# Optimization experiments

Measured on AMD Instinct MI355X. Metric: run time of the kernel, lower is better.

## Reference

```python
import jax, jax.numpy as jnp
import numpy as np

BEV_H, BEV_W, BEV_Z = 100, 100, 4
PC_RANGE = (-51.2, -51.2, -5.0, 51.2, 51.2, 3.0)
EPS = 1e-5
N_CAM, C_DIM, H_IMG, W_IMG, BATCH = 6, 256, 32, 88, 1


def _make_lidar2img(n_cam, h_img, w_img):
    # Realistic rig: n_cam cameras at equal yaw spacing, ~70 deg HFOV,
    # intrinsics expressed in feature-map pixel units.
    fx = w_img / (2.0 * np.tan(np.deg2rad(35.0)))
    fy = fx
    cx, cy = w_img / 2.0, h_img / 2.0
    K = np.array([[fx, 0, cx, 0], [0, fy, cy, 0], [0, 0, 1, 0], [0, 0, 0, 1]], np.float32)
    mats = []
    for i in range(n_cam):
        th = 2.0 * np.pi * i / n_cam
        c, s = np.cos(th), np.sin(th)
        # camera: z forward (world yaw th), x right, y down; camera at ego origin
        R = np.array([[-s, c, 0.0], [0.0, 0.0, -1.0], [c, s, 0.0]], np.float32)
        T = np.eye(4, dtype=np.float32)
        T[:3, :3] = R
        mats.append(K @ T)
    return np.stack(mats)[None]  # (1, n_cam, 4, 4)


def get_reference_points(H, W, Z, bs):
    ref_y, ref_x = jnp.meshgrid(
        jnp.linspace(0.5, H - 0.5, H, dtype=jnp.float32),
        jnp.linspace(0.5, W - 0.5, W, dtype=jnp.float32), indexing='ij')
    ref_y = (ref_y.reshape(-1) / H)[None, :, None]          # (1, HW, 1)
    ref_x = (ref_x.reshape(-1) / W)[None, :, None]
    ref_x = jnp.broadcast_to(ref_x, (1, H * W, Z))
    ref_y = jnp.broadcast_to(ref_y, (1, H * W, Z))
    ref_z = jnp.broadcast_to(jnp.linspace(0.5, Z - 0.5, Z, dtype=jnp.float32)[None, None, :], (1, H * W, Z))
    ref_3d = jnp.stack((ref_x, ref_y, ref_z), -1)           # (1, HW, Z, 3)
    return jnp.broadcast_to(ref_3d, (bs, H * W, Z, 3))


def bilinear_sample(img, gx, gy):
    # img: (BN, C, H, W); gx, gy in [-1, 1]: (BN, P)
    # F.grid_sample bilinear, padding_mode='zeros', align_corners=False
    BN, C, H, W = img.shape
    x = (gx + 1.0) * W * 0.5 - 0.5
    y = (gy + 1.0) * H * 0.5 - 0.5
    x0 = jnp.floor(x)
    y0 = jnp.floor(y)
    wx1 = x - x0
    wy1 = y - y0
    flat = img.reshape(BN, C, H * W)

    def corner(xi, yi, w):
        valid = (xi >= 0) & (xi < W) & (yi >= 0) & (yi < H)
        xc = jnp.clip(xi, 0, W - 1).astype(jnp.int32)
        yc = jnp.clip(yi, 0, H - 1).astype(jnp.int32)
        idx = yc * W + xc                                   # (BN, P)
        idx = jnp.broadcast_to(idx[:, None, :], (BN, C, idx.shape[-1]))
        vals = jnp.take_along_axis(flat, idx, axis=2)       # (BN, C, P)
        return vals * (w * valid.astype(img.dtype))[:, None, :]

    out = corner(x0, y0, (1 - wx1) * (1 - wy1))
    out = out + corner(x0 + 1, y0, wx1 * (1 - wy1))
    out = out + corner(x0, y0 + 1, (1 - wx1) * wy1)
    out = out + corner(x0 + 1, y0 + 1, wx1 * wy1)
    return out


def setup_inputs() -> dict:
    key = jax.random.key(0)
    k0, k1, k2, k3 = jax.random.split(key, 4)
    Nq = BEV_H * BEV_W
    query = jax.random.normal(k0, (BATCH, Nq, C_DIM), jnp.float32)
    img_feats = jax.random.normal(k1, (BATCH, N_CAM, C_DIM, H_IMG, W_IMG), jnp.float32)
    lidar2img = jnp.asarray(_make_lidar2img(N_CAM, H_IMG, W_IMG))
    W_out = jax.random.normal(k2, (C_DIM, C_DIM), jnp.float32) * 0.02
    b_out = jax.random.normal(k3, (C_DIM,), jnp.float32) * 0.02
    return {'query': query, 'img_feats': img_feats, 'lidar2img': lidar2img,
            'W_out': W_out, 'b_out': b_out}


def reference(query, img_feats, lidar2img, W_out, b_out):
    B, Nq, C = query.shape
    N_cam, _, H_img, W_img = img_feats.shape[1], img_feats.shape[2], img_feats.shape[3], img_feats.shape[4]
    Z = BEV_Z
    pc = PC_RANGE

    ref = get_reference_points(BEV_H, BEV_W, Z, B)          # (B, Nq, Z, 3) normalized
    ref = jnp.stack([
        ref[..., 0] * (pc[3] - pc[0]) + pc[0],
        ref[..., 1] * (pc[4] - pc[1]) + pc[1],
        ref[..., 2] * (pc[5] - pc[2]) + pc[2],
    ], axis=-1)
    pts = jnp.concatenate([ref, jnp.ones_like(ref[..., :1])], -1)  # (B, Nq, Z, 4)
    pts = pts.reshape(B, Nq * Z, 4)
    # project: (B, N_cam, P, 4)
    cam = jnp.einsum('bnij,bpj->bnpi', lidar2img, pts)
    z = cam[..., 2:3]
    mask = z > EPS
    xy = cam[..., 0:2] / jnp.maximum(z, EPS)
    gx = (xy[..., 0] / W_img - 0.5) * 2.0                    # (B, N_cam, P)
    gy = (xy[..., 1] / H_img - 0.5) * 2.0
    mask = (mask[..., 0] & (gx > -1.0) & (gx < 1.0) & (gy > -1.0) & (gy < 1.0))

    img_flat = img_feats.reshape(B * N_cam, C, H_img, W_img)
    sampled = bilinear_sample(img_flat, gx.reshape(B * N_cam, -1), gy.reshape(B * N_cam, -1))
    sampled = sampled.reshape(B, N_cam, C, Nq, Z)
    sampled = jnp.nan_to_num(sampled * mask.reshape(B, N_cam, 1, Nq, Z).astype(sampled.dtype))

    w = jnp.mean(sampled, axis=1)                            # (B, C, Nq, Z) mean over cams
    w = jnp.mean(w, axis=3)                                  # (B, C, Nq) mean over Z
    out = jnp.transpose(w, (0, 2, 1))                        # (B, Nq, C)
    return out @ W_out.T + b_out + query
```

## Files before the change

### kernel.cpp

```cpp
#include <hip/hip_runtime.h>
#include <hip/hip_bf16.h>
#include <math.h>

#define BEV_H 100
#define BEV_W 100
#define BEV_Z 4
#define N_CAM 6
#define C_DIM 256
#define H_IMG 32
#define W_IMG 88
#define NQ (BEV_H * BEV_W)
#define HW_IMG (H_IMG * W_IMG)

typedef float f32x4 __attribute__((ext_vector_type(4)));
typedef short short8 __attribute__((ext_vector_type(8)));

__device__ __forceinline__ unsigned short f2b(float f) {
    __hip_bfloat16 h = __float2bfloat16(f);
    return *reinterpret_cast<unsigned short*>(&h);
}
__device__ __forceinline__ float b2f_lo(unsigned int u) {
    return __uint_as_float(u << 16);
}
__device__ __forceinline__ float b2f_hi(unsigned int u) {
    return __uint_as_float(u & 0xffff0000u);
}

__device__ __forceinline__ int xcd_swz(int bid, int nwg) {
    int q = nwg >> 3, r = nwg & 7;
    int xcd = bid & 7;
    int idx = bid >> 3;
    int base = (xcd < r) ? xcd * (q + 1) : r * (q + 1) + (xcd - r) * q;
    return base + idx;
}

__global__ __launch_bounds__(256) void prep_kernel(const float* __restrict__ img,
                                                   const float* __restrict__ Wout,
                                                   unsigned short* __restrict__ imgT,
                                                   unsigned short* __restrict__ Woutb) {
    int cam = blockIdx.z;
    int t = threadIdx.x;
    if (cam == N_CAM) {
        if (blockIdx.y == 0 && blockIdx.x < 64) {
            int base = (blockIdx.x * 256 + t) * 4;
            float4 v = *(const float4*)(Wout + base);
            ushort4 o;
            o.x = f2b(v.x); o.y = f2b(v.y); o.z = f2b(v.z); o.w = f2b(v.w);
            *(ushort4*)(Woutb + base) = o;
        }
        return;
    }
    __shared__ unsigned short tile[32][68];
    int hw0 = blockIdx.x * 32;
    int c0  = blockIdx.y * 64;
    const float* src = img + (size_t)cam * C_DIM * HW_IMG;
    #pragma unroll
    for (int i = 0; i < 2; ++i) {
        int e = i * 256 + t;
        int c  = e >> 3;
        int hq = e & 7;
        float4 v = *(const float4*)(src + (size_t)(c0 + c) * HW_IMG + hw0 + hq * 4);
        tile[hq * 4 + 0][c] = f2b(v.x);
        tile[hq * 4 + 1][c] = f2b(v.y);
        tile[hq * 4 + 2][c] = f2b(v.z);
        tile[hq * 4 + 3][c] = f2b(v.w);
    }
    __syncthreads();
    unsigned short* dst = imgT + (size_t)cam * HW_IMG * C_DIM;
    #pragma unroll
    for (int i = 0; i < 2; ++i) {
        int e = i * 256 + t;
        int hw = e >> 4;
        int cq = e & 15;
        ushort4 o;
        o.x = tile[hw][cq * 4 + 0];
        o.y = tile[hw][cq * 4 + 1];
        o.z = tile[hw][cq * 4 + 2];
        o.w = tile[hw][cq * 4 + 3];
        *(ushort4*)(dst + (size_t)(hw0 + hw) * C_DIM + c0 + cq * 4) = o;
    }
}

__global__ __launch_bounds__(256) void sample_kernel(const unsigned short* __restrict__ imgT,
                                                     const float* __restrict__ l2i,
                                                     unsigned short* __restrict__ wbuf) {
    __shared__ int   ent_off[8][24][4];
    __shared__ float ent_w[8][24][4];
    __shared__ int   counts[8];
    int t = threadIdx.x;
    int blk = xcd_swz(blockIdx.x, NQ / 8);

    {
        int ql   = t >> 5;
        int slot = t & 31;
        int q = blk * 8 + ql;
        int ix = q % BEV_W;
        int iy = q / BEV_W;
        float x = ((ix + 0.5f) / (float)BEV_W) * 102.4f - 51.2f;
        float y = ((iy + 0.5f) / (float)BEV_H) * 102.4f - 51.2f;

        bool valid = false;
        int   o0 = 0, o1 = 0, o2 = 0, o3 = 0;
        float w0 = 0.f, w1 = 0.f, w2 = 0.f, w3 = 0.f;
        if (slot < 24) {
            int cam = slot >> 2;
            int zi  = slot & 3;
            const float* L = l2i + cam * 16;
            float zl = (zi + 0.5f) * 8.0f - 5.0f;
            float cx = fmaf(L[0], x, fmaf(L[1], y, fmaf(L[2],  zl, L[3])));
            float cy = fmaf(L[4], x, fmaf(L[5], y, fmaf(L[6],  zl, L[7])));
            float cz = fmaf(L[8], x, fmaf(L[9], y, fmaf(L[10], zl, L[11])));
            float denom = fmaxf(cz, 1e-5f);
            float inv = __builtin_amdgcn_rcpf(denom);
            float u = cx * inv;
            float v = cy * inv;
            if ((cz > 1e-5f) && (u > 0.f) && (u < (float)W_IMG)
                             && (v > 0.f) && (v < (float)H_IMG)) {
                valid = true;
                float xs = u - 0.5f;
                float ys = v - 0.5f;
                float x0f = floorf(xs), y0f = floorf(ys);
                float wx1 = xs - x0f,   wy1 = ys - y0f;
                float wx0 = 1.0f - wx1, wy0 = 1.0f - wy1;
                int x0 = (int)x0f, y0 = (int)y0f;
                int x1 = x0 + 1,   y1 = y0 + 1;
                float mxl = (x0 >= 0)     ? 1.f : 0.f;
                float mxh = (x1 < W_IMG)  ? 1.f : 0.f;
                float myl = (y0 >= 0)     ? 1.f : 0.f;
                float myh = (y1 < H_IMG)  ? 1.f : 0.f;
                int x0c = max(x0, 0), x1c = min(x1, W_IMG - 1);
                int y0c = max(y0, 0), y1c = min(y1, H_IMG - 1);
                int cbase = cam * HW_IMG;
                o0 = (cbase + y0c * W_IMG + x0c) << 9;  w0 = (wx0 * mxl) * (wy0 * myl);
                o1 = (cbase + y0c * W_IMG + x1c) << 9;  w1 = (wx1 * mxh) * (wy0 * myl);
                o2 = (cbase + y1c * W_IMG + x0c) << 9;  w2 = (wx0 * mxl) * (wy1 * myh);
                o3 = (cbase + y1c * W_IMG + x1c) << 9;  w3 = (wx1 * mxh) * (wy1 * myh);
            }
        }
        unsigned long long bal = __ballot(valid);
        unsigned int half = (t & 32) ? (unsigned int)(bal >> 32) : (unsigned int)bal;
        int lane32 = t & 31;
        int pre = __popc(half & ((1u << lane32) - 1u));
        if (valid) {
            ent_off[ql][pre][0] = o0; ent_off[ql][pre][1] = o1;
            ent_off[ql][pre][2] = o2; ent_off[ql][pre][3] = o3;
            ent_w[ql][pre][0] = w0; ent_w[ql][pre][1] = w1;
            ent_w[ql][pre][2] = w2; ent_w[ql][pre][3] = w3;
        }
        if (lane32 == 0) counts[ql] = __popc(half);
    }
    __syncthreads();

    int qi = t >> 5;
    int lane32 = t & 31;
    int q = blk * 8 + qi;
    int cnt = counts[qi];
    const char* base = (const char*)imgT + lane32 * 16;

    float a0 = 0.f, a1 = 0.f, a2 = 0.f, a3 = 0.f;
    float a4 = 0.f, a5 = 0.f, a6 = 0.f, a7 = 0.f;
    for (int i = 0; i < cnt; ++i) {
        int4   offs = *(const int4*)(&ent_off[qi][i][0]);
        float4 wv   = *(const float4*)(&ent_w[qi][i][0]);
        int4 f0 = *(const int4*)(base + offs.x);
        int4 f1 = *(const int4*)(base + offs.y);
        int4 f2 = *(const int4*)(base + offs.z);
        int4 f3 = *(const int4*)(base + offs.w);
        a0 += b2f_lo(f0.x) * wv.x; a1 += b2f_hi(f0.x) * wv.x;
        a2 += b2f_lo(f0.y) * wv.x; a3 += b2f_hi(f0.y) * wv.x;
        a4 += b2f_lo(f0.z) * wv.x; a5 += b2f_hi(f0.z) * wv.x;
        a6 += b2f_lo(f0.w) * wv.x; a7 += b2f_hi(f0.w) * wv.x;
        a0 += b2f_lo(f1.x) * wv.y; a1 += b2f_hi(f1.x) * wv.y;
        a2 += b2f_lo(f1.y) * wv.y; a3 += b2f_hi(f1.y) * wv.y;
        a4 += b2f_lo(f1.z) * wv.y; a5 += b2f_hi(f1.z) * wv.y;
        a6 += b2f_lo(f1.w) * wv.y; a7 += b2f_hi(f1.w) * wv.y;
        a0 += b2f_lo(f2.x) * wv.z; a1 += b2f_hi(f2.x) * wv.z;
        a2 += b2f_lo(f2.y) * wv.z; a3 += b2f_hi(f2.y) * wv.z;
        a4 += b2f_lo(f2.z) * wv.z; a5 += b2f_hi(f2.z) * wv.z;
        a6 += b2f_lo(f2.w) * wv.z; a7 += b2f_hi(f2.w) * wv.z;
        a0 += b2f_lo(f3.x) * wv.w; a1 += b2f_hi(f3.x) * wv.w;
        a2 += b2f_lo(f3.y) * wv.w; a3 += b2f_hi(f3.y) * wv.w;
        a4 += b2f_lo(f3.z) * wv.w; a5 += b2f_hi(f3.z) * wv.w;
        a6 += b2f_lo(f3.w) * wv.w; a7 += b2f_hi(f3.w) * wv.w;
    }
    const float s = 1.0f / 24.0f;
    int4 o;
    o.x = (int)f2b(a0 * s) | ((int)f2b(a1 * s) << 16);
    o.y = (int)f2b(a2 * s) | ((int)f2b(a3 * s) << 16);
    o.z = (int)f2b(a4 * s) | ((int)f2b(a5 * s) << 16);
    o.w = (int)f2b(a6 * s) | ((int)f2b(a7 * s) << 16);
    *(int4*)(wbuf + (size_t)q * C_DIM + lane32 * 8) = o;
}

#define BM 64
#define BN 64
#define BKK 128
__global__ __launch_bounds__(256) void gemm_kernel(const unsigned short* __restrict__ A,
                                                   const unsigned short* __restrict__ B,
                                                   const float* __restrict__ bout,
                                                   const float* __restrict__ query,
                                                   float* __restrict__ out) {
    __shared__ unsigned short Al[BM * BKK];
    __shared__ unsigned short Bl[BN * BKK];
    int blk = xcd_swz(blockIdx.x, 157 * 4);
    int rb = (blk >> 2) * BM;
    int cb = (blk & 3) * BN;
    int t = threadIdx.x;
    int lane = t & 63;
    int wid = t >> 6;
    int wr = wid >> 1, wc = wid & 1;
    int fr = lane & 15;
    int kq = lane >> 4;

    f32x4 acc[2][2] = {};

    for (int kt = 0; kt < C_DIM; kt += BKK) {
        #pragma unroll
        for (int i = 0; i < 4; ++i) {
            int idx = i * 256 + t;
            int row = idx >> 4;
            int ch  = idx & 15;
            int4 av = make_int4(0, 0, 0, 0);
            int grow = rb + row;
            if (grow < NQ) av = *(const int4*)(A + (size_t)grow * C_DIM + kt + ch * 8);
            int4 bv = *(const int4*)(B + (size_t)(cb + row) * C_DIM + kt + ch * 8);
            int off = (row * 256 + ch * 16) ^ ((row & 7) << 4);
            *(int4*)((char*)Al + off) = av;
            *(int4*)((char*)Bl + off) = bv;
        }
        __syncthreads();

        #pragma unroll
        for (int ks = 0; ks < 4; ++ks) {
            int kbyte = ks * 64 + kq * 16;
            int ra0 = wr * 32 + fr, ra1 = ra0 + 16;
            int rb0 = wc * 32 + fr, rb1 = rb0 + 16;
            short8 af0 = *(const short8*)((const char*)Al + ((ra0 * 256 + kbyte) ^ ((ra0 & 7) << 4)));
            short8 af1 = *(const short8*)((const char*)Al + ((ra1 * 256 + kbyte) ^ ((ra1 & 7) << 4)));
            short8 bf0 = *(const short8*)((const char*)Bl + ((rb0 * 256 + kbyte) ^ ((rb0 & 7) << 4)));
            short8 bf1 = *(const short8*)((const char*)Bl + ((rb1 * 256 + kbyte) ^ ((rb1 & 7) << 4)));
            acc[0][0] = __builtin_amdgcn_mfma_f32_16x16x32_bf16(af0, bf0, acc[0][0], 0, 0, 0);
            acc[0][1] = __builtin_amdgcn_mfma_f32_16x16x32_bf16(af0, bf1, acc[0][1], 0, 0, 0);
            acc[1][0] = __builtin_amdgcn_mfma_f32_16x16x32_bf16(af1, bf0, acc[1][0], 0, 0, 0);
            acc[1][1] = __builtin_amdgcn_mfma_f32_16x16x32_bf16(af1, bf1, acc[1][1], 0, 0, 0);
        }
        __syncthreads();
    }

    int crow = (lane >> 4) * 4;
    int ccol = lane & 15;
    #pragma unroll
    for (int fi = 0; fi < 2; ++fi) {
        #pragma unroll
        for (int fj = 0; fj < 2; ++fj) {
            int n = cb + wc * 32 + fj * 16 + ccol;
            float bn = bout[n];
            #pragma unroll
            for (int r = 0; r < 4; ++r) {
                int m = rb + wr * 32 + fi * 16 + crow + r;
                if (m < NQ) {
                    size_t off = (size_t)m * C_DIM + n;
                    out[off] = acc[fi][fj][r] + bn + query[off];
                }
            }
        }
    }
}

extern "C" void kernel_launch(void* const* d_in, const int* in_sizes, int n_in,
                              void* d_out, int out_size, void* d_ws, size_t ws_size,
                              hipStream_t stream) {
    const float* query = (const float*)d_in[0];
    const float* img   = (const float*)d_in[1];
    const float* l2i   = (const float*)d_in[2];
    const float* Wout  = (const float*)d_in[3];
    const float* bout  = (const float*)d_in[4];
    float* out = (float*)d_out;

    unsigned short* imgT  = (unsigned short*)d_ws;
    unsigned short* wbuf  = (unsigned short*)((char*)d_ws + 8650752);
    unsigned short* Woutb = (unsigned short*)((char*)d_ws + 13770752);

    dim3 gP(HW_IMG / 32, C_DIM / 64, N_CAM + 1);
    prep_kernel<<<gP, 256, 0, stream>>>(img, Wout, imgT, Woutb);

    sample_kernel<<<NQ / 8, 256, 0, stream>>>(imgT, l2i, wbuf);

    gemm_kernel<<<157 * 4, 256, 0, stream>>>(wbuf, Woutb, bout, query, out);
}
```

Before: 27.95 us.

## Fuse bilinear sampling with the output projection GEMM in one kernel

Merges the sample kernel and the GEMM kernel. Each block now handles 32 queries, builds the sampled bf16 row tile directly in LDS, then loops over the four 64-column output chunks with MFMA, staging Wout through LDS. This removes the intermediate wbuf round trip through global memory and one kernel launch. In exchange each block uses much more LDS (about 72 KB), the grid drops to 313 blocks, and every block reloads all of Wout, so occupancy and parallelism may suffer.

New measurement: 35.04 us. 1.25x slower.

```diff
diff --git a/kernel.cpp b/kernel.cpp
--- a/kernel.cpp
+++ b/kernel.cpp
@@ -11,6 +11,8 @@
 #define W_IMG 88
 #define NQ (BEV_H * BEV_W)
 #define HW_IMG (H_IMG * W_IMG)
+#define QB 32
+#define NBLK ((NQ + QB - 1) / QB)
 
 typedef float f32x4 __attribute__((ext_vector_type(4)));
 typedef short short8 __attribute__((ext_vector_type(8)));
@@ -81,19 +83,26 @@
     }
 }
 
-__global__ __launch_bounds__(256) void sample_kernel(const unsigned short* __restrict__ imgT,
-                                                     const float* __restrict__ l2i,
-                                                     unsigned short* __restrict__ wbuf) {
-    __shared__ int   ent_off[8][24][4];
-    __shared__ float ent_w[8][24][4];
-    __shared__ int   counts[8];
+__global__ __launch_bounds__(256) void fused_kernel(const unsigned short* __restrict__ imgT,
+                                                    const float* __restrict__ l2i,
+                                                    const unsigned short* __restrict__ Woutb,
+                                                    const float* __restrict__ bout,
+                                                    const float* __restrict__ query,
+                                                    float* __restrict__ out) {
+    __shared__ int   ent_off[QB][24][4];
+    __shared__ float ent_w[QB][24][4];
+    __shared__ int   counts[QB];
+    __shared__ unsigned short Atile[QB * C_DIM];
+    __shared__ unsigned short Btile[64 * C_DIM];
     int t = threadIdx.x;
-    int blk = xcd_swz(blockIdx.x, NQ / 8);
-
-    {
-        int ql   = t >> 5;
+    int blk = xcd_swz(blockIdx.x, NBLK);
+    int qbase = blk * QB;
+
+    #pragma unroll
+    for (int pass = 0; pass < 4; ++pass) {
+        int ql   = pass * 8 + (t >> 5);
         int slot = t & 31;
-        int q = blk * 8 + ql;
+        int q = qbase + ql;
         int ix = q % BEV_W;
         int iy = q / BEV_W;
         float x = ((ix + 0.5f) / (float)BEV_W) * 102.4f - 51.2f;
@@ -102,7 +111,7 @@
         bool valid = false;
         int   o0 = 0, o1 = 0, o2 = 0, o3 = 0;
         float w0 = 0.f, w1 = 0.f, w2 = 0.f, w3 = 0.f;
-        if (slot < 24) {
+        if (slot < 24 && q < NQ) {
             int cam = slot >> 2;
             int zi  = slot & 3;
             const float* L = l2i + cam * 16;
@@ -151,119 +160,99 @@
     }
     __syncthreads();
 
-    int qi = t >> 5;
-    int lane32 = t & 31;
-    int q = blk * 8 + qi;
-    int cnt = counts[qi];
-    const char* base = (const char*)imgT + lane32 * 16;
-
-    float a0 = 0.f, a1 = 0.f, a2 = 0.f, a3 = 0.f;
-    float a4 = 0.f, a5 = 0.f, a6 = 0.f, a7 = 0.f;
-    for (int i = 0; i < cnt; ++i) {
-        int4   offs = *(const int4*)(&ent_off[qi][i][0]);
-        float4 wv   = *(const float4*)(&ent_w[qi][i][0]);
-        int4 f0 = *(const int4*)(base + offs.x);
-        int4 f1 = *(const int4*)(base + offs.y);
-        int4 f2 = *(const int4*)(base + offs.z);
-        int4 f3 = *(const int4*)(base + offs.w);
-        a0 += b2f_lo(f0.x) * wv.x; a1 += b2f_hi(f0.x) * wv.x;
-        a2 += b2f_lo(f0.y) * wv.x; a3 += b2f_hi(f0.y) * wv.x;
-        a4 += b2f_lo(f0.z) * wv.x; a5 += b2f_hi(f0.z) * wv.x;
-        a6 += b2f_lo(f0.w) * wv.x; a7 += b2f_hi(f0.w) * wv.x;
-        a0 += b2f_lo(f1.x) * wv.y; a1 += b2f_hi(f1.x) * wv.y;
-        a2 += b2f_lo(f1.y) * wv.y; a3 += b2f_hi(f1.y) * wv.y;
-        a4 += b2f_lo(f1.z) * wv.y; a5 += b2f_hi(f1.z) * wv.y;
-        a6 += b2f_lo(f1.w) * wv.y; a7 += b2f_hi(f1.w) * wv.y;
-        a0 += b2f_lo(f2.x) * wv.z; a1 += b2f_hi(f2.x) * wv.z;
-        a2 += b2f_lo(f2.y) * wv.z; a3 += b2f_hi(f2.y) * wv.z;
-        a4 += b2f_lo(f2.z) * wv.z; a5 += b2f_hi(f2.z) * wv.z;
-        a6 += b2f_lo(f2.w) * wv.z; a7 += b2f_hi(f2.w) * wv.z;
-        a0 += b2f_lo(f3.x) * wv.w; a1 += b2f_hi(f3.x) * wv.w;
-        a2 += b2f_lo(f3.y) * wv.w; a3 += b2f_hi(f3.y) * wv.w;
-        a4 += b2f_lo(f3.z) * wv.w; a5 += b2f_hi(f3.z) * wv.w;
-        a6 += b2f_lo(f3.w) * wv.w; a7 += b2f_hi(f3.w) * wv.w;
-    }
-    const float s = 1.0f / 24.0f;
-    int4 o;
-    o.x = (int)f2b(a0 * s) | ((int)f2b(a1 * s) << 16);
-    o.y = (int)f2b(a2 * s) | ((int)f2b(a3 * s) << 16);
-    o.z = (int)f2b(a4 * s) | ((int)f2b(a5 * s) << 16);
-    o.w = (int)f2b(a6 * s) | ((int)f2b(a7 * s) << 16);
-    *(int4*)(wbuf + (size_t)q * C_DIM + lane32 * 8) = o;
-}
-
-#define BM 64
-#define BN 64
-#define BKK 128
-__global__ __launch_bounds__(256) void gemm_kernel(const unsigned short* __restrict__ A,
-                                                   const unsigned short* __restrict__ B,
-                                                   const float* __restrict__ bout,
-                                                   const float* __restrict__ query,
-                                                   float* __restrict__ out) {
-    __shared__ unsigned short Al[BM * BKK];
-    __shared__ unsigned short Bl[BN * BKK];
-    int blk = xcd_swz(blockIdx.x, 157 * 4);
-    int rb = (blk >> 2) * BM;
-    int cb = (blk & 3) * BN;
-    int t = threadIdx.x;
+    {
+        int hw = t >> 5;
+        int lane32 = t & 31;
+        const char* base = (const char*)imgT + lane32 * 16;
+        #pragma unroll
+        for (int p = 0; p < 4; ++p) {
+            int ql = p * 8 + hw;
+            int cnt = counts[ql];
+            float a0 = 0.f, a1 = 0.f, a2 = 0.f, a3 = 0.f;
+            float a4 = 0.f, a5 = 0.f, a6 = 0.f, a7 = 0.f;
+            for (int i = 0; i < cnt; ++i) {
+                int4   offs = *(const int4*)(&ent_off[ql][i][0]);
+                float4 wv   = *(const float4*)(&ent_w[ql][i][0]);
+                int4 f0 = *(const int4*)(base + offs.x);
+                int4 f1 = *(const int4*)(base + offs.y);
+                int4 f2 = *(const int4*)(base + offs.z);
+                int4 f3 = *(const int4*)(base + offs.w);
+                a0 += b2f_lo(f0.x) * wv.x; a1 += b2f_hi(f0.x) * wv.x;
+                a2 += b2f_lo(f0.y) * wv.x; a3 += b2f_hi(f0.y) * wv.x;
+                a4 += b2f_lo(f0.z) * wv.x; a5 += b2f_hi(f0.z) * wv.x;
+                a6 += b2f_lo(f0.w) * wv.x; a7 += b2f_hi(f0.w) * wv.x;
+                a0 += b2f_lo(f1.x) * wv.y; a1 += b2f_hi(f1.x) * wv.y;
+                a2 += b2f_lo(f1.y) * wv.y; a3 += b2f_hi(f1.y) * wv.y;
+                a4 += b2f_lo(f1.z) * wv.y; a5 += b2f_hi(f1.z) * wv.y;
+                a6 += b2f_lo(f1.w) * wv.y; a7 += b2f_hi(f1.w) * wv.y;
+                a0 += b2f_lo(f2.x) * wv.z; a1 += b2f_hi(f2.x) * wv.z;
+                a2 += b2f_lo(f2.y) * wv.z; a3 += b2f_hi(f2.y) * wv.z;
+                a4 += b2f_lo(f2.z) * wv.z; a5 += b2f_hi(f2.z) * wv.z;
+                a6 += b2f_lo(f2.w) * wv.z; a7 += b2f_hi(f2.w) * wv.z;
+                a0 += b2f_lo(f3.x) * wv.w; a1 += b2f_hi(f3.x) * wv.w;
+                a2 += b2f_lo(f3.y) * wv.w; a3 += b2f_hi(f3.y) * wv.w;
+                a4 += b2f_lo(f3.z) * wv.w; a5 += b2f_hi(f3.z) * wv.w;
+                a6 += b2f_lo(f3.w) * wv.w; a7 += b2f_hi(f3.w) * wv.w;
+            }
+            const float s = 1.0f / 24.0f;
+            int4 o;
+            o.x = (int)f2b(a0 * s) | ((int)f2b(a1 * s) << 16);
+            o.y = (int)f2b(a2 * s) | ((int)f2b(a3 * s) << 16);
+            o.z = (int)f2b(a4 * s) | ((int)f2b(a5 * s) << 16);
+            o.w = (int)f2b(a6 * s) | ((int)f2b(a7 * s) << 16);
+            int off = (ql * 512 + lane32 * 16) ^ ((ql & 7) << 4);
+            *(int4*)((char*)Atile + off) = o;
+        }
+    }
+    __syncthreads();
+
     int lane = t & 63;
     int wid = t >> 6;
-    int wr = wid >> 1, wc = wid & 1;
     int fr = lane & 15;
     int kq = lane >> 4;
-
-    f32x4 acc[2][2] = {};
-
-    for (int kt = 0; kt < C_DIM; kt += BKK) {
-        #pragma unroll
-        for (int i = 0; i < 4; ++i) {
+    int crow = kq * 4;
+    int ccol = fr;
+
+    for (int cb = 0; cb < C_DIM; cb += 64) {
+        #pragma unroll
+        for (int i = 0; i < 8; ++i) {
             int idx = i * 256 + t;
-            int row = idx >> 4;
-            int ch  = idx & 15;
-            int4 av = make_int4(0, 0, 0, 0);
-            int grow = rb + row;
-            if (grow < NQ) av = *(const int4*)(A + (size_t)grow * C_DIM + kt + ch * 8);
-            int4 bv = *(const int4*)(B + (size_t)(cb + row) * C_DIM + kt + ch * 8);
-            int off = (row * 256 + ch * 16) ^ ((row & 7) << 4);
-            *(int4*)((char*)Al + off) = av;
-            *(int4*)((char*)Bl + off) = bv;
+            int row = idx >> 5;
+            int ch  = idx & 31;
+            int4 bv = *(const int4*)(Woutb + (size_t)(cb + row) * C_DIM + ch * 8);
+            int off = (row * 512 + ch * 16) ^ ((row & 7) << 4);
+            *(int4*)((char*)Btile + off) = bv;
         }
         __syncthreads();
 
-        #pragma unroll
-        for (int ks = 0; ks < 4; ++ks) {
+        f32x4 acc0 = {}, acc1 = {};
+        #pragma unroll
+        for (int ks = 0; ks < 8; ++ks) {
             int kbyte = ks * 64 + kq * 16;
-            int ra0 = wr * 32 + fr, ra1 = ra0 + 16;
-            int rb0 = wc * 32 + fr, rb1 = rb0 + 16;
-            short8 af0 = *(const short8*)((const char*)Al + ((ra0 * 256 + kbyte) ^ ((ra0 & 7) << 4)));
-            short8 af1 = *(const short8*)((const char*)Al + ((ra1 * 256 + kbyte) ^ ((ra1 & 7) << 4)));
-            short8 bf0 = *(const short8*)((const char*)Bl + ((rb0 * 256 + kbyte) ^ ((rb0 & 7) << 4)));
-            short8 bf1 = *(const short8*)((const char*)Bl + ((rb1 * 256 + kbyte) ^ ((rb1 & 7) << 4)));
-            acc[0][0] = __builtin_amdgcn_mfma_f32_16x16x32_bf16(af0, bf0, acc[0][0], 0, 0, 0);
-            acc[0][1] = __builtin_amdgcn_mfma_f32_16x16x32_bf16(af0, bf1, acc[0][1], 0, 0, 0);
-            acc[1][0] = __builtin_amdgcn_mfma_f32_16x16x32_bf16(af1, bf0, acc[1][0], 0, 0, 0);
-            acc[1][1] = __builtin_amdgcn_mfma_f32_16x16x32_bf16(af1, bf1, acc[1][1], 0, 0, 0);
-        }
-        __syncthreads();
-    }
-
-    int crow = (lane >> 4) * 4;
-    int ccol = lane & 15;
-    #pragma unroll
-    for (int fi = 0; fi < 2; ++fi) {
-        #pragma unroll
-        for (int fj = 0; fj < 2; ++fj) {
-            int n = cb + wc * 32 + fj * 16 + ccol;
-            float bn = bout[n];
+            int m0 = fr, m1 = fr + 16;
+            int n = wid * 16 + fr;
+            short8 af0 = *(const short8*)((const char*)Atile + ((m0 * 512 + kbyte) ^ ((m0 & 7) << 4)));
+            short8 af1 = *(const short8*)((const char*)Atile + ((m1 * 512 + kbyte) ^ ((m1 & 7) << 4)));
+            short8 bf  = *(const short8*)((const char*)Btile + ((n  * 512 + kbyte) ^ ((n  & 7) << 4)));
+            acc0 = __builtin_amdgcn_mfma_f32_16x16x32_bf16(af0, bf, acc0, 0, 0, 0);
+            acc1 = __builtin_amdgcn_mfma_f32_16x16x32_bf16(af1, bf, acc1, 0, 0, 0);
+        }
+
+        int nn = cb + wid * 16 + ccol;
+        float bn = bout[nn];
+        #pragma unroll
+        for (int fi = 0; fi < 2; ++fi) {
+            f32x4 a = fi ? acc1 : acc0;
             #pragma unroll
             for (int r = 0; r < 4; ++r) {
-                int m = rb + wr * 32 + fi * 16 + crow + r;
+                int m = qbase + fi * 16 + crow + r;
                 if (m < NQ) {
-                    size_t off = (size_t)m * C_DIM + n;
-                    out[off] = acc[fi][fj][r] + bn + query[off];
+                    size_t off = (size_t)m * C_DIM + nn;
+                    out[off] = a[r] + bn + query[off];
                 }
             }
         }
+        __syncthreads();
     }
 }
 
@@ -278,13 +267,10 @@
     float* out = (float*)d_out;
 
     unsigned short* imgT  = (unsigned short*)d_ws;
-    unsigned short* wbuf  = (unsigned short*)((char*)d_ws + 8650752);
-    unsigned short* Woutb = (unsigned short*)((char*)d_ws + 13770752);
+    unsigned short* Woutb = (unsigned short*)((char*)d_ws + 8650752);
 
     dim3 gP(HW_IMG / 32, C_DIM / 64, N_CAM + 1);
     prep_kernel<<<gP, 256, 0, stream>>>(img, Wout, imgT, Woutb);
 
-    sample_kernel<<<NQ / 8, 256, 0, stream>>>(imgT, l2i, wbuf);
-
-    gemm_kernel<<<157 * 4, 256, 0, stream>>>(wbuf, Woutb, bout, query, out);
-}
+    fused_kernel<<<NBLK, 256, 0, stream>>>(imgT, l2i, Woutb, bout, query, out);
+}
```
